# Optimization experiments

Measured on AMD Instinct MI355X. Metric: run time of the kernel, lower is better.

The kernel has to match this reference:

```python
import jax, jax.numpy as jnp
import numpy as np
from jax import lax

D_MODEL, D_STATE, D_CONV, D_INNER, DT_RANK = 1024, 16, 4, 2048, 64
B_SZ, L_SEQ = 2, 4096

def setup_inputs() -> dict:
    key = jax.random.key(0)
    ks = jax.random.split(key, 12)
    s = 0.02
    x = jax.random.normal(ks[0], (B_SZ, L_SEQ, D_MODEL), jnp.float32)
    norm_w = jnp.ones((D_MODEL,), jnp.float32)
    norm_b = jnp.zeros((D_MODEL,), jnp.float32)
    W_in = jax.random.normal(ks[1], (D_MODEL, 2 * D_INNER), jnp.float32) * s
    conv_w = jax.random.normal(ks[2], (D_INNER, 1, D_CONV), jnp.float32) * 0.5
    conv_b = jnp.zeros((D_INNER,), jnp.float32)
    W_x = jax.random.normal(ks[3], (D_INNER, DT_RANK + 2 * D_STATE), jnp.float32) * s
    W_dt = jax.random.normal(ks[4], (DT_RANK, D_INNER), jnp.float32) * s
    # dt bias init as in the torch module: inverse-softplus of dt in [dt_min, dt_max]
    dt_init = jnp.exp(jax.random.uniform(ks[5], (D_INNER,)) * (np.log(0.1) - np.log(0.001)) + np.log(0.001))
    dt_init = jnp.clip(dt_init, 1e-4, None)
    b_dt = dt_init + jnp.log(-jnp.expm1(-dt_init))
    A_log = jnp.log(jnp.broadcast_to(jnp.arange(1, D_STATE + 1, dtype=jnp.float32)[None, :], (D_INNER, D_STATE)))
    D = jnp.ones((D_INNER,), jnp.float32)
    W_out = jax.random.normal(ks[6], (D_INNER, D_MODEL), jnp.float32) * s
    return {"x": x, "norm_w": norm_w, "norm_b": norm_b, "W_in": W_in,
            "conv_w": conv_w, "conv_b": conv_b, "W_x": W_x, "W_dt": W_dt,
            "b_dt": b_dt, "A_log": A_log, "D": D, "W_out": W_out}

def _silu(v):
    return v * jax.nn.sigmoid(v)

def _layernorm(v, w, b, eps=1e-5):
    mu = jnp.mean(v, axis=-1, keepdims=True)
    var = jnp.var(v, axis=-1, keepdims=True)
    return (v - mu) * lax.rsqrt(var + eps) * w + b

def _selective_scan(u, delta, A, Bm, Cm, Dp):
    # u, delta: [B,L,d_inner]; A: [d_inner,N]; Bm, Cm: [B,L,N]; Dp: [d_inner]
    Bb, L, d_inner = u.shape
    N = A.shape[1]

    def step(h, inp):
        dt_t, u_t, B_t, C_t = inp  # [B,d_inner],[B,d_inner],[B,N],[B,N]
        A_bar = jnp.exp(dt_t[..., None] * A)                       # [B,d_inner,N]
        h = A_bar * h + dt_t[..., None] * B_t[:, None, :] * u_t[..., None]
        y = jnp.sum(h * C_t[:, None, :], axis=-1)                  # [B,d_inner]
        return h, y

    h0 = jnp.zeros((Bb, d_inner, N), u.dtype)
    xs = (jnp.swapaxes(delta, 0, 1), jnp.swapaxes(u, 0, 1),
          jnp.swapaxes(Bm, 0, 1), jnp.swapaxes(Cm, 0, 1))
    _, ys = lax.scan(step, h0, xs)          # ys: [L,B,d_inner]
    y = jnp.swapaxes(ys, 0, 1)
    return y + u * Dp[None, None, :]

def reference(x, norm_w, norm_b, W_in, conv_w, conv_b, W_x, W_dt, b_dt, A_log, D, W_out):
    residual = x
    xn = _layernorm(x, norm_w, norm_b)
    xz = xn @ W_in                                      # [B,L,2*d_inner]
    x_ssm, z = jnp.split(xz, 2, axis=-1)
    # depthwise causal conv1d (torch pads both sides then truncates -> left pad)
    xt = jnp.swapaxes(x_ssm, 1, 2)                      # [B,d_inner,L]
    xt = jnp.pad(xt, ((0, 0), (0, 0), (D_CONV - 1, 0)))
    xc = lax.conv_general_dilated(xt, conv_w, window_strides=(1,), padding='VALID',
                                  feature_group_count=D_INNER,
                                  dimension_numbers=('NCH', 'OIH', 'NCH'))
    xc = xc + conv_b[None, :, None]
    x_conv = jnp.swapaxes(_silu(xc), 1, 2)              # [B,L,d_inner]
    x_dbl = x_conv @ W_x                                # [B,L,dt_rank+2N]
    dt_low, B_mat, C_mat = jnp.split(x_dbl, [DT_RANK, DT_RANK + D_STATE], axis=-1)
    delta = jax.nn.softplus(dt_low @ W_dt + b_dt)       # [B,L,d_inner]
    A = -jnp.exp(A_log)
    y = _selective_scan(x_conv, delta, A, B_mat, C_mat, D)
    y = y * _silu(z)
    return residual + y @ W_out
```

## Files before the change

### kernel.cpp

```cpp
#include <hip/hip_runtime.h>

typedef unsigned short u16;
typedef __attribute__((ext_vector_type(8))) __bf16 bf16x8;
typedef __attribute__((ext_vector_type(4))) float f32x4;

#define LSEQ 4096
#define DMODEL 1024
#define DINNER 2048

__device__ __forceinline__ float bf2f(u16 u) {
  union { unsigned u; float f; } v; v.u = ((unsigned)u) << 16; return v.f;
}
__device__ __forceinline__ u16 f2bf(float f) {
  union { float f; unsigned u; } v; v.f = f;
  unsigned r = v.u + 0x7fffu + ((v.u >> 16) & 1u);
  return (u16)(r >> 16);
}
__device__ __forceinline__ void gload_lds16(const void* g, void* l) {
  __builtin_amdgcn_global_load_lds(
      (__attribute__((address_space(1))) void*)(unsigned long long)g,
      (__attribute__((address_space(3))) void*)(unsigned int)(unsigned long long)l,
      16, 0, 0);
}
__device__ __forceinline__ float sigmoidf_(float v) { return 1.f / (1.f + __expf(-v)); }

__global__ __launch_bounds__(256) void ln_kernel(const float* __restrict__ x,
                                                 const float* __restrict__ w,
                                                 const float* __restrict__ b,
                                                 u16* __restrict__ out) {
  int row = blockIdx.x;
  const float* xr = x + (size_t)row * DMODEL;
  int t = threadIdx.x;
  float4 v = ((const float4*)xr)[t];
  float s = v.x + v.y + v.z + v.w;
  float s2 = v.x * v.x + v.y * v.y + v.z * v.z + v.w * v.w;
  for (int off = 32; off; off >>= 1) {
    s += __shfl_down(s, off);
    s2 += __shfl_down(s2, off);
  }
  __shared__ float ls[4], ls2[4];
  int wid = t >> 6;
  if ((t & 63) == 0) { ls[wid] = s; ls2[wid] = s2; }
  __syncthreads();
  s = ls[0] + ls[1] + ls[2] + ls[3];
  s2 = ls2[0] + ls2[1] + ls2[2] + ls2[3];
  float mu = s * (1.f / DMODEL);
  float var = s2 * (1.f / DMODEL) - mu * mu;
  float rs = rsqrtf(var + 1e-5f);
  float4 wv = ((const float4*)w)[t];
  float4 bv = ((const float4*)b)[t];
  unsigned p0 = (unsigned)f2bf((v.x - mu) * rs * wv.x + bv.x) |
                ((unsigned)f2bf((v.y - mu) * rs * wv.y + bv.y) << 16);
  unsigned p1 = (unsigned)f2bf((v.z - mu) * rs * wv.z + bv.z) |
                ((unsigned)f2bf((v.w - mu) * rs * wv.w + bv.w) << 16);
  ((uint2*)(out + (size_t)row * DMODEL))[t] = make_uint2(p0, p1);
}

__global__ __launch_bounds__(256) void tc_kernel(const float* __restrict__ in,
                                                 u16* __restrict__ out,
                                                 int K, int N, int Npad) {
  __shared__ float tile[32][33];
  int n0 = blockIdx.x * 32, k0 = blockIdx.y * 32;
  int tx = threadIdx.x & 31, ty = threadIdx.x >> 5;
  for (int i = ty; i < 32; i += 8) {
    int k = k0 + i, n = n0 + tx;
    tile[i][tx] = (k < K && n < N) ? in[(size_t)k * N + n] : 0.f;
  }
  __syncthreads();
  for (int i = ty; i < 32; i += 8) {
    int n = n0 + i, k = k0 + tx;
    if (n < Npad && k < K) out[(size_t)n * K + k] = f2bf(tile[tx][i]);
  }
}

template <int OUT_BF16, int EPI, int SPLITK>
__global__ __launch_bounds__(256) void gemm_bt(const u16* __restrict__ A,
                                               const u16* __restrict__ Bt,
                                               void* __restrict__ Cout,
                                               const float* __restrict__ aux,
                                               int M, int N, int K, int ld, int cthresh) {
  __shared__ alignas(16) u16 As[128 * 32];
  __shared__ alignas(16) u16 Bs[128 * 32];
  int t = threadIdx.x;
  int w = t >> 6, ln = t & 63;
  int wr = w >> 1, wc = w & 1;
  int bm = blockIdx.y, bn = blockIdx.x;
  int lr = ln & 15, lk = (ln >> 4) * 8;
  f32x4 acc[4][4] = {};
  int kz = SPLITK ? blockIdx.z * K : 0;
  const u16* Abase = A + (size_t)bm * 128 * ld + kz;
  const u16* Bbase = Bt + (size_t)bn * 128 * ld + kz;
  for (int k0 = 0; k0 < K; k0 += 32) {
#pragma unroll
    for (int c = 0; c < 2; ++c) {
      int chunk = w * 2 + c;
      int ee = chunk * 512 + ln * 8;
      int row = ee >> 5, col = ee & 31;
      gload_lds16(Abase + (size_t)row * ld + k0 + col, As + chunk * 512);
      gload_lds16(Bbase + (size_t)row * ld + k0 + col, Bs + chunk * 512);
    }
    __syncthreads();
    bf16x8 af[4], bfr[4];
#pragma unroll
    for (int m = 0; m < 4; ++m)
      af[m] = *(const bf16x8*)(As + (wr * 64 + m * 16 + lr) * 32 + lk);
#pragma unroll
    for (int n = 0; n < 4; ++n)
      bfr[n] = *(const bf16x8*)(Bs + (wc * 64 + n * 16 + lr) * 32 + lk);
#pragma unroll
    for (int m = 0; m < 4; ++m)
#pragma unroll
      for (int n = 0; n < 4; ++n)
        acc[m][n] = __builtin_amdgcn_mfma_f32_16x16x32_bf16(af[m], bfr[n], acc[m][n], 0, 0, 0);
    __syncthreads();
  }
  int rb = bm * 128 + wr * 64 + (ln >> 4) * 4;
  int cb = bn * 128 + wc * 64 + lr;
  float* Cpart = SPLITK ? ((float*)Cout + (size_t)blockIdx.z * M * N) : (float*)Cout;
#pragma unroll
  for (int m = 0; m < 4; ++m)
#pragma unroll
    for (int n = 0; n < 4; ++n)
#pragma unroll
      for (int r = 0; r < 4; ++r) {
        int row = rb + m * 16 + r;
        int col = cb + n * 16;
        float v = acc[m][n][r];
        if (EPI == 1) v += aux[(size_t)row * N + col];
        if (EPI == 2 && col >= cthresh) v = v * sigmoidf_(v);
        if (EPI == 3) {
          float dtr = v + aux[col];
          v = dtr > 15.f ? dtr : __logf(1.f + __expf(dtr));
        }
        if (OUT_BF16)
          ((u16*)Cpart)[(size_t)row * N + col] = f2bf(v);
        else
          Cpart[(size_t)row * N + col] = v;
      }
}

__global__ __launch_bounds__(256) void reduce_xdbl(const float* __restrict__ part,
                                                   float* __restrict__ xdbl,
                                                   u16* __restrict__ dtlow) {
  int i = blockIdx.x * 256 + threadIdx.x;
  float s = 0.f;
#pragma unroll
  for (int z = 0; z < 8; ++z) s += part[(size_t)z * (8192 * 128) + i];
  xdbl[i] = s;
  int col = i & 127;
  if (col < 64) dtlow[(size_t)(i >> 7) * 64 + col] = f2bf(s);
}

__global__ __launch_bounds__(256) void conv_silu(const u16* __restrict__ xz,
                                                 const float* __restrict__ cw,
                                                 const float* __restrict__ cb,
                                                 u16* __restrict__ out) {
  int d = blockIdx.x * 256 + threadIdx.x;
  int l0 = blockIdx.y * 8;
  int b = blockIdx.z;
  float w0 = cw[d * 4 + 0], w1 = cw[d * 4 + 1], w2 = cw[d * 4 + 2], w3 = cw[d * 4 + 3];
  float bias = cb[d];
  const u16* xp = xz + ((size_t)b * LSEQ) * 4096 + d;
  float xv[11];
#pragma unroll
  for (int i = 0; i < 11; ++i) {
    int l = l0 - 3 + i;
    xv[i] = (l >= 0) ? bf2f(xp[(size_t)l * 4096]) : 0.f;
  }
  u16* op = out + ((size_t)b * LSEQ + l0) * DINNER + d;
#pragma unroll
  for (int i = 0; i < 8; ++i) {
    float acc = bias + w0 * xv[i] + w1 * xv[i + 1] + w2 * xv[i + 2] + w3 * xv[i + 3];
    float sv = acc * sigmoidf_(acc);
    op[(size_t)i * DINNER] = f2bf(sv);
  }
}

__device__ __forceinline__ void compute_a(float dt, const float* An, bool fast, float* av) {
  if (fast) {
    float q = __expf(-dt);
    float q2 = q * q, q4 = q2 * q2;
    av[0] = q; av[1] = q2; av[2] = q2 * q; av[3] = q4;
#pragma unroll
    for (int n = 4; n < 16; ++n) av[n] = av[n - 4] * q4;
  } else {
#pragma unroll
    for (int n = 0; n < 16; ++n) av[n] = __expf(dt * An[n]);
  }
}

__global__ __launch_bounds__(256) void scan1(const u16* __restrict__ dtbf,
                                             const u16* __restrict__ ubf,
                                             const float* __restrict__ xdbl,
                                             const float* __restrict__ A_log,
                                             float* __restrict__ P,
                                             float* __restrict__ H) {
  int d = blockIdx.x * 256 + threadIdx.x;
  int b = blockIdx.y, c = blockIdx.z;
  size_t row0 = (size_t)b * LSEQ + c * 64;
  float An[16];
  bool fast = true;
  {
    const float4* A4 = (const float4*)(A_log + (size_t)d * 16);
#pragma unroll
    for (int q = 0; q < 4; ++q) {
      float4 a = A4[q];
      An[q * 4 + 0] = -__expf(a.x);
      An[q * 4 + 1] = -__expf(a.y);
      An[q * 4 + 2] = -__expf(a.z);
      An[q * 4 + 3] = -__expf(a.w);
    }
#pragma unroll
    for (int n = 0; n < 16; ++n)
      fast = fast && (__builtin_fabsf(An[n] + (float)(n + 1)) < 1e-3f * (n + 1));
  }
  const u16* dtp = dtbf + row0 * DINNER + d;
  const u16* up = ubf + row0 * DINNER + d;
  const float* Bp = xdbl + row0 * 128 + 64;
  float h[16];
#pragma unroll
  for (int n = 0; n < 16; ++n) h[n] = 0.f;
  float sdt = 0.f;
#pragma unroll 2
  for (int i = 0; i < 64; ++i) {
    float dt = bf2f(dtp[(size_t)i * DINNER]);
    float uu = bf2f(up[(size_t)i * DINNER]);
    float dtu = dt * uu;
    sdt += dt;
    const float4* B4 = (const float4*)(Bp + (size_t)i * 128);
    float4 b0 = B4[0], b1 = B4[1], b2 = B4[2], b3 = B4[3];
    float Bf[16] = {b0.x, b0.y, b0.z, b0.w, b1.x, b1.y, b1.z, b1.w,
                    b2.x, b2.y, b2.z, b2.w, b3.x, b3.y, b3.z, b3.w};
    float av[16];
    compute_a(dt, An, fast, av);
#pragma unroll
    for (int n = 0; n < 16; ++n) h[n] = av[n] * h[n] + dtu * Bf[n];
  }
  size_t idx = (size_t)c * 65536 + ((size_t)b * DINNER + d) * 16;
  float4* P4 = (float4*)(P + idx);
  float4* H4 = (float4*)(H + idx);
#pragma unroll
  for (int q = 0; q < 4; ++q) {
    P4[q] = make_float4(__expf(An[q * 4 + 0] * sdt), __expf(An[q * 4 + 1] * sdt),
                        __expf(An[q * 4 + 2] * sdt), __expf(An[q * 4 + 3] * sdt));
    H4[q] = make_float4(h[q * 4], h[q * 4 + 1], h[q * 4 + 2], h[q * 4 + 3]);
  }
}

__global__ __launch_bounds__(256) void scan2(const float* __restrict__ P,
                                             const float* __restrict__ H,
                                             float* __restrict__ Hinit) {
  int i = blockIdx.x * 256 + threadIdx.x;
  float h = 0.f;
  for (int c = 0; c < 64; ++c) {
    Hinit[(size_t)c * 65536 + i] = h;
    h = P[(size_t)c * 65536 + i] * h + H[(size_t)c * 65536 + i];
  }
}

__global__ __launch_bounds__(256) void scan3(const u16* __restrict__ dtbf,
                                             const u16* __restrict__ ubf,
                                             const float* __restrict__ xdbl,
                                             const float* __restrict__ A_log,
                                             const float* __restrict__ Dp,
                                             const u16* __restrict__ xzbf,
                                             const float* __restrict__ Hinit,
                                             u16* __restrict__ ybf) {
  int d = blockIdx.x * 256 + threadIdx.x;
  int b = blockIdx.y, c = blockIdx.z;
  size_t row0 = (size_t)b * LSEQ + c * 64;
  float An[16];
  bool fast = true;
  {
    const float4* A4 = (const float4*)(A_log + (size_t)d * 16);
#pragma unroll
    for (int q = 0; q < 4; ++q) {
      float4 a = A4[q];
      An[q * 4 + 0] = -__expf(a.x);
      An[q * 4 + 1] = -__expf(a.y);
      An[q * 4 + 2] = -__expf(a.z);
      An[q * 4 + 3] = -__expf(a.w);
    }
#pragma unroll
    for (int n = 0; n < 16; ++n)
      fast = fast && (__builtin_fabsf(An[n] + (float)(n + 1)) < 1e-3f * (n + 1));
  }
  const u16* dtp = dtbf + row0 * DINNER + d;
  const u16* up = ubf + row0 * DINNER + d;
  const float* Bp = xdbl + row0 * 128 + 64;
  const float* Cp = xdbl + row0 * 128 + 80;
  const u16* gp = xzbf + row0 * 4096 + DINNER + d;
  u16* yp = ybf + row0 * DINNER + d;
  float Dv = Dp[d];
  float h[16];
  {
    const float4* Hi4 = (const float4*)(Hinit + (size_t)c * 65536 + ((size_t)b * DINNER + d) * 16);
#pragma unroll
    for (int q = 0; q < 4; ++q) {
      float4 hv = Hi4[q];
      h[q * 4 + 0] = hv.x; h[q * 4 + 1] = hv.y; h[q * 4 + 2] = hv.z; h[q * 4 + 3] = hv.w;
    }
  }
#pragma unroll 2
  for (int i = 0; i < 64; ++i) {
    float dt = bf2f(dtp[(size_t)i * DINNER]);
    float uu = bf2f(up[(size_t)i * DINNER]);
    float dtu = dt * uu;
    const float4* B4 = (const float4*)(Bp + (size_t)i * 128);
    float4 b0 = B4[0], b1 = B4[1], b2 = B4[2], b3 = B4[3];
    float Bf[16] = {b0.x, b0.y, b0.z, b0.w, b1.x, b1.y, b1.z, b1.w,
                    b2.x, b2.y, b2.z, b2.w, b3.x, b3.y, b3.z, b3.w};
    const float4* C4 = (const float4*)(Cp + (size_t)i * 128);
    float4 c0 = C4[0], c1 = C4[1], c2 = C4[2], c3 = C4[3];
    float Cf[16] = {c0.x, c0.y, c0.z, c0.w, c1.x, c1.y, c1.z, c1.w,
                    c2.x, c2.y, c2.z, c2.w, c3.x, c3.y, c3.z, c3.w};
    float av[16];
    compute_a(dt, An, fast, av);
    float y = 0.f;
#pragma unroll
    for (int n = 0; n < 16; ++n) {
      h[n] = av[n] * h[n] + dtu * Bf[n];
      y += h[n] * Cf[n];
    }
    float g = bf2f(gp[(size_t)i * 4096]);
    yp[(size_t)i * DINNER] = f2bf((y + uu * Dv) * g);
  }
}

extern "C" void kernel_launch(void* const* d_in, const int* in_sizes, int n_in,
                              void* d_out, int out_size, void* d_ws, size_t ws_size,
                              hipStream_t stream) {
  const float* x = (const float*)d_in[0];
  const float* nw = (const float*)d_in[1];
  const float* nb = (const float*)d_in[2];
  const float* W_in = (const float*)d_in[3];
  const float* convw = (const float*)d_in[4];
  const float* convb = (const float*)d_in[5];
  const float* W_x = (const float*)d_in[6];
  const float* W_dt = (const float*)d_in[7];
  const float* b_dt = (const float*)d_in[8];
  const float* A_log = (const float*)d_in[9];
  const float* Dp = (const float*)d_in[10];
  const float* W_out = (const float*)d_in[11];
  float* out = (float*)d_out;

  char* wp = (char*)d_ws;
  auto alloc = [&](size_t bytes) {
    char* p = wp;
    wp += (bytes + 255) & ~(size_t)255;
    return p;
  };
  u16* xz_bf = (u16*)alloc((size_t)8192 * 4096 * 2);
  u16* xconv_bf = (u16*)alloc((size_t)8192 * 2048 * 2);
  u16* xn_bf = (u16*)alloc((size_t)8192 * 1024 * 2);
  float* xdbl = (float*)alloc((size_t)8192 * 128 * 4);
  u16* dt_bf = (u16*)alloc((size_t)8192 * 2048 * 2);
  u16* dtlow_bf = (u16*)alloc((size_t)8192 * 64 * 2);
  u16* Wint = (u16*)alloc((size_t)4096 * 1024 * 2);
  u16* Wxt = (u16*)alloc((size_t)128 * 2048 * 2);
  u16* Wdtt = (u16*)alloc((size_t)2048 * 64 * 2);
  u16* Woutt = (u16*)alloc((size_t)1024 * 2048 * 2);
  float* P = (float*)alloc((size_t)64 * 65536 * 4);
  float* H = (float*)alloc((size_t)64 * 65536 * 4);
  float* Hinit = (float*)alloc((size_t)64 * 65536 * 4);
  float* xdbl_part = (float*)P;
  u16* y_bf = (u16*)P;

  tc_kernel<<<dim3(128, 32), 256, 0, stream>>>(W_in, Wint, 1024, 4096, 4096);
  tc_kernel<<<dim3(4, 64), 256, 0, stream>>>(W_x, Wxt, 2048, 96, 128);
  tc_kernel<<<dim3(64, 2), 256, 0, stream>>>(W_dt, Wdtt, 64, 2048, 2048);
  tc_kernel<<<dim3(32, 64), 256, 0, stream>>>(W_out, Woutt, 2048, 1024, 1024);

  ln_kernel<<<8192, 256, 0, stream>>>(x, nw, nb, xn_bf);
  gemm_bt<1, 2, 0><<<dim3(32, 64), 256, 0, stream>>>(xn_bf, Wint, xz_bf, nullptr,
                                                     8192, 4096, 1024, 1024, 2048);
  conv_silu<<<dim3(8, 512, 2), 256, 0, stream>>>(xz_bf, convw, convb, xconv_bf);
  gemm_bt<0, 0, 1><<<dim3(1, 64, 8), 256, 0, stream>>>(xconv_bf, Wxt, xdbl_part, nullptr,
                                                       8192, 128, 256, 2048, 0);
  reduce_xdbl<<<4096, 256, 0, stream>>>(xdbl_part, xdbl, dtlow_bf);
  gemm_bt<1, 3, 0><<<dim3(16, 64), 256, 0, stream>>>(dtlow_bf, Wdtt, dt_bf, b_dt,
                                                     8192, 2048, 64, 64, 0);
  scan1<<<dim3(8, 2, 64), 256, 0, stream>>>(dt_bf, xconv_bf, xdbl, A_log, P, H);
  scan2<<<256, 256, 0, stream>>>(P, H, Hinit);
  scan3<<<dim3(8, 2, 64), 256, 0, stream>>>(dt_bf, xconv_bf, xdbl, A_log, Dp, xz_bf,
                                            Hinit, y_bf);
  gemm_bt<0, 1, 0><<<dim3(8, 64), 256, 0, stream>>>(y_bf, Woutt, out, x,
                                                    8192, 1024, 2048, 2048, 0);
}
```

Measured before the change: 362.7 us.

## Add 256x256 pipelined 8-wave GEMM for in-proj and out-proj

Adds a new GEMM kernel with 512 threads and 256x256 output tiles. It uses a 64-wide K step, an XOR-swizzled LDS layout and double-buffered direct global-to-LDS loads. Loads for later K tiles are interleaved with quarter-tile MFMA groups under s_setprio, to raise data reuse and overlap memory with compute on the two large projection GEMMs. The kernel uses 128KB of LDS, and the out-proj launches only 128 blocks, which may underfill the GPU. The old kernel's EPI 1/2 epilogue paths are removed since only EPI 3 still uses it.

New measurement: 346.4 us. 1.05x faster.

```diff
diff --git a/kernel.cpp b/kernel.cpp
--- a/kernel.cpp
+++ b/kernel.cpp
@@ -71,6 +71,123 @@
     int n = n0 + i, k = k0 + tx;
     if (n < Npad && k < K) out[(size_t)n * K + k] = f2bf(tile[tx][i]);
   }
+}
+
+__device__ __forceinline__ void stage8(const u16* grow0, int ld, int kcol0,
+                                       u16* lds_u, int ln) {
+  int rr = ln >> 3, kb = ln & 7;
+  gload_lds16(grow0 + (size_t)rr * ld + kcol0 + ((kb ^ rr) << 3), lds_u);
+}
+
+#define LDA_FRAGS(mh, buf)                                                         \
+  _Pragma("unroll") for (int mf = 0; mf < 4; ++mf)                                 \
+  _Pragma("unroll") for (int kk = 0; kk < 2; ++kk)                                 \
+    a[mf][kk] = *(const bf16x8*)(LA + (buf) * 16384 +                              \
+        (wm * 128 + (mh) * 64 + mf * 16 + lr) * 64 + (((kk * 4 + lq) ^ key) << 3));
+
+#define LDB_FRAGS(nh, buf)                                                         \
+  _Pragma("unroll") for (int nf = 0; nf < 2; ++nf)                                 \
+  _Pragma("unroll") for (int kk = 0; kk < 2; ++kk)                                 \
+    bb[nh][nf][kk] = *(const bf16x8*)(LB + (buf) * 16384 +                         \
+        (wn * 64 + (nh) * 32 + nf * 16 + lr) * 64 + (((kk * 4 + lq) ^ key) << 3));
+
+#define MFMA_Q(mh, nh)                                                             \
+  __builtin_amdgcn_s_setprio(1);                                                   \
+  _Pragma("unroll") for (int mf = 0; mf < 4; ++mf)                                 \
+  _Pragma("unroll") for (int nf = 0; nf < 2; ++nf)                                 \
+  _Pragma("unroll") for (int kk = 0; kk < 2; ++kk)                                 \
+    acc[(mh) * 4 + mf][(nh) * 2 + nf] = __builtin_amdgcn_mfma_f32_16x16x32_bf16(   \
+        a[mf][kk], bb[nh][nf][kk], acc[(mh) * 4 + mf][(nh) * 2 + nf], 0, 0, 0);    \
+  __builtin_amdgcn_s_setprio(0);
+
+#define STAGE_A(unit, kt, buf)                                                     \
+  _Pragma("unroll") for (int c = 0; c < 2; ++c) {                                  \
+    int g = w * 2 + c;                                                             \
+    int r0 = ((g < 8) ? g * 8 : (g - 8) * 8 + 128) + (unit) * 64;                  \
+    stage8(Ag + (size_t)r0 * K, K, (kt) * 64, LA + (buf) * 16384 + r0 * 64, ln);   \
+  }
+
+#define STAGE_B(half, kt, buf)                                                     \
+  _Pragma("unroll") for (int c = 0; c < 2; ++c) {                                  \
+    int g = w * 2 + c;                                                             \
+    int r0 = (g >> 2) * 64 + (half) * 32 + (g & 3) * 8;                            \
+    stage8(Bg + (size_t)r0 * K, K, (kt) * 64, LB + (buf) * 16384 + r0 * 64, ln);   \
+  }
+
+template <int OUT_BF16, int EPI>
+__global__ __launch_bounds__(512, 2) void gemm8p(const u16* __restrict__ A,
+                                                 const u16* __restrict__ Bt,
+                                                 void* __restrict__ Cout,
+                                                 const float* __restrict__ aux,
+                                                 int M, int N, int K, int cthresh) {
+  __shared__ alignas(16) u16 lds[65536];
+  u16* LA = lds;
+  u16* LB = lds + 32768;
+  int t = threadIdx.x;
+  int w = t >> 6, ln = t & 63;
+  int wm = w >> 2, wn = w & 3;
+  int bm = blockIdx.y, bn = blockIdx.x;
+  int lr = ln & 15, lq = ln >> 4, key = ln & 7;
+  int NT = K >> 6;
+  const u16* Ag = A + (size_t)bm * 256 * K;
+  const u16* Bg = Bt + (size_t)bn * 256 * K;
+  f32x4 acc[8][4] = {};
+  bf16x8 a[4][2], bb[2][2][2];
+
+  STAGE_A(0, 0, 0); STAGE_B(0, 0, 0); STAGE_B(1, 0, 0); STAGE_A(1, 0, 0);
+  int k1 = NT > 1 ? 1 : 0;
+  STAGE_A(0, k1, 1); STAGE_B(0, k1, 1); STAGE_B(1, k1, 1);
+  asm volatile("s_waitcnt vmcnt(6)" ::: "memory");
+  __builtin_amdgcn_s_barrier();
+
+  for (int T = 0; T < NT; ++T) {
+    int b0 = T & 1, b1 = b0 ^ 1;
+    int kt1 = (T + 1 < NT) ? T + 1 : NT - 1;
+    int kt2 = (T + 2 < NT) ? T + 2 : NT - 1;
+    LDA_FRAGS(0, b0);
+    LDB_FRAGS(0, b0);
+    STAGE_A(1, kt1, b1);
+    __builtin_amdgcn_s_barrier();
+    asm volatile("s_waitcnt lgkmcnt(0)" ::: "memory");
+    MFMA_Q(0, 0);
+    __builtin_amdgcn_s_barrier();
+    LDB_FRAGS(1, b0);
+    STAGE_A(0, kt2, b0);
+    __builtin_amdgcn_s_barrier();
+    asm volatile("s_waitcnt lgkmcnt(0)" ::: "memory");
+    MFMA_Q(0, 1);
+    __builtin_amdgcn_s_barrier();
+    LDA_FRAGS(1, b0);
+    STAGE_B(0, kt2, b0);
+    __builtin_amdgcn_s_barrier();
+    asm volatile("s_waitcnt lgkmcnt(0)" ::: "memory");
+    MFMA_Q(1, 1);
+    __builtin_amdgcn_s_barrier();
+    STAGE_B(1, kt2, b0);
+    asm volatile("s_waitcnt vmcnt(6)" ::: "memory");
+    __builtin_amdgcn_s_barrier();
+    MFMA_Q(1, 0);
+    __builtin_amdgcn_s_barrier();
+  }
+
+  int crow0 = bm * 256 + wm * 128;
+  int ccol0 = bn * 256 + wn * 64;
+#pragma unroll
+  for (int mf = 0; mf < 8; ++mf)
+#pragma unroll
+    for (int nf = 0; nf < 4; ++nf)
+#pragma unroll
+      for (int r = 0; r < 4; ++r) {
+        int row = crow0 + mf * 16 + lq * 4 + r;
+        int col = ccol0 + nf * 16 + lr;
+        float v = acc[mf][nf][r];
+        if (EPI == 1) v += aux[(size_t)row * N + col];
+        if (EPI == 2 && col >= cthresh) v = v * sigmoidf_(v);
+        if (OUT_BF16)
+          ((u16*)Cout)[(size_t)row * N + col] = f2bf(v);
+        else
+          ((float*)Cout)[(size_t)row * N + col] = v;
+      }
 }
 
 template <int OUT_BF16, int EPI, int SPLITK>
@@ -126,8 +243,6 @@
         int row = rb + m * 16 + r;
         int col = cb + n * 16;
         float v = acc[m][n][r];
-        if (EPI == 1) v += aux[(size_t)row * N + col];
-        if (EPI == 2 && col >= cthresh) v = v * sigmoidf_(v);
         if (EPI == 3) {
           float dtr = v + aux[col];
           v = dtr > 15.f ? dtr : __logf(1.f + __expf(dtr));
@@ -372,8 +487,8 @@
   tc_kernel<<<dim3(32, 64), 256, 0, stream>>>(W_out, Woutt, 2048, 1024, 1024);
 
   ln_kernel<<<8192, 256, 0, stream>>>(x, nw, nb, xn_bf);
-  gemm_bt<1, 2, 0><<<dim3(32, 64), 256, 0, stream>>>(xn_bf, Wint, xz_bf, nullptr,
-                                                     8192, 4096, 1024, 1024, 2048);
+  gemm8p<1, 2><<<dim3(16, 32), 512, 0, stream>>>(xn_bf, Wint, xz_bf, nullptr,
+                                                 8192, 4096, 1024, 2048);
   conv_silu<<<dim3(8, 512, 2), 256, 0, stream>>>(xz_bf, convw, convb, xconv_bf);
   gemm_bt<0, 0, 1><<<dim3(1, 64, 8), 256, 0, stream>>>(xconv_bf, Wxt, xdbl_part, nullptr,
                                                        8192, 128, 256, 2048, 0);
@@ -384,6 +499,6 @@
   scan2<<<256, 256, 0, stream>>>(P, H, Hinit);
   scan3<<<dim3(8, 2, 64), 256, 0, stream>>>(dt_bf, xconv_bf, xdbl, A_log, Dp, xz_bf,
                                             Hinit, y_bf);
-  gemm_bt<0, 1, 0><<<dim3(8, 64), 256, 0, stream>>>(y_bf, Woutt, out, x,
-                                                    8192, 1024, 2048, 2048, 0);
-}
+  gemm8p<0, 1><<<dim3(4, 32), 512, 0, stream>>>(y_bf, Woutt, out, x,
+                                                8192, 1024, 2048, 0);
+}
```
